# Performance work log

Measured on AMD Instinct MI355X. Metric: run time of the kernel, lower is better.

## Reference

```python
import jax, jax.numpy as jnp
import numpy as np

B, S, D, H = 4, 2048, 512, 8
INNER = D  # assumed AttentionHead.inner_size == size (naive single-head attention)


def setup_inputs() -> dict:
    key = jax.random.key(0)
    ks = jax.random.split(key, 8)
    scale = 0.02
    return {
        "emb_input": jax.random.normal(ks[0], (B, S, D), dtype=jnp.float32),
        "Wq": jax.random.normal(ks[1], (H, D, INNER), dtype=jnp.float32) * scale,
        "bq": jnp.zeros((H, INNER), dtype=jnp.float32),
        "Wk": jax.random.normal(ks[2], (H, D, INNER), dtype=jnp.float32) * scale,
        "bk": jnp.zeros((H, INNER), dtype=jnp.float32),
        "Wv": jax.random.normal(ks[3], (H, D, INNER), dtype=jnp.float32) * scale,
        "bv": jnp.zeros((H, INNER), dtype=jnp.float32),
        "Wp": jax.random.normal(ks[4], (H * INNER, D), dtype=jnp.float32) * scale,
        "bp": jnp.zeros((D,), dtype=jnp.float32),
    }


def reference(emb_input, Wq, bq, Wk, bk, Wv, bv, Wp, bp):
    # All heads batched into one einsum instead of a Python loop over submodules.
    x = emb_input  # [B, S, D]
    q = jnp.einsum("bsd,hde->bhse", x, Wq) + bq[None, :, None, :]  # [B,H,S,E]
    k = jnp.einsum("bsd,hde->bhse", x, Wk) + bk[None, :, None, :]
    v = jnp.einsum("bsd,hde->bhse", x, Wv) + bv[None, :, None, :]
    scores = jnp.einsum("bhse,bhte->bhst", q, k) / jnp.sqrt(
        jnp.asarray(INNER, dtype=x.dtype)
    )  # [B,H,S,S]
    attn = jax.nn.softmax(scores, axis=-1)
    o = jnp.einsum("bhst,bhte->bhse", attn, v)  # [B,H,S,E]
    # concat over heads (dim=2 in torch => feature dim after per-head outputs)
    o = jnp.transpose(o, (0, 2, 1, 3)).reshape(B, S, H * INNER)
    return o @ Wp + bp  # [B, S, D]
```

## Files before the change

kernel.cpp:

```cpp
#include <hip/hip_runtime.h>


typedef short s8v __attribute__((ext_vector_type(8)));
typedef float f4v __attribute__((ext_vector_type(4)));
typedef unsigned short us;
typedef us us4v __attribute__((ext_vector_type(4)));

__device__ inline us f2b(float f) {
  union { float f; unsigned u; } v; v.f = f;
  unsigned r = v.u + 0x7FFFu + ((v.u >> 16) & 1u);
  return (us)(r >> 16);
}

__device__ inline void gld16(const us* g, us* l) {
  __builtin_amdgcn_global_load_lds(
      (const __attribute__((address_space(1))) void*)g,
      (__attribute__((address_space(3))) void*)l, 16, 0, 0);
}

template <int EPI>
__global__ __launch_bounds__(512, 4) void gemm_nt(
    const us* __restrict__ A, int lda, long long sA0, long long sA1,
    const us* __restrict__ Bm, int ldb, long long sB0, long long sB1,
    const float* __restrict__ bias, const float* __restrict__ bias2,
    const float* __restrict__ bias3,
    void* __restrict__ Cv, void* __restrict__ C2, void* __restrict__ C3,
    int ldc, long long sC0, long long sC1,
    int K, float alpha, int L, int sbits) {
  __shared__ us As[2][8192];
  __shared__ us Bs[2][4096];
  const int t = threadIdx.x;
  const int wv = t >> 6, ln = t & 63;
  const int m16 = ln & 15, quad = ln >> 4;

  const int gx = gridDim.x, gxy = gx * gridDim.y;
  const int nblk = gxy * gridDim.z;
  const int flat = blockIdx.x + gx * blockIdx.y + gxy * blockIdx.z;
  int nid = flat;
  if ((nblk & 7) == 0) nid = (flat & 7) * (nblk >> 3) + (flat >> 3);
  const int bz = nid / gxy, rem = nid % gxy;
  const int by = rem / gx, bx = rem % gx;

  const long long row0 = (long long)by * 256;
  const long long col0 = (long long)bx * 128;
  const int zo = bz >> L, zi = bz & ((1 << L) - 1);
  const us* Az = A + zo * sA0 + zi * sA1;
  const us* Bz = Bm + zo * sB0 + zi * sB1;

  int offA[2], offB;
#pragma unroll
  for (int j = 0; j < 2; ++j) {
    const int c = t + 512 * j;
    const int mb = c >> 6, qd = (c >> 4) & 3, mm = c & 15;
    offA[j] = (int)((row0 + mb * 16 + mm) * (long long)lda + qd * 8);
  }
  {
    const int mb = t >> 6, qd = (t >> 4) & 3, mm = t & 15;
    offB = (int)((col0 + mb * 16 + mm) * (long long)ldb + qd * 8);
  }

  f4v acc[4][4];
#pragma unroll
  for (int r = 0; r < 4; ++r)
#pragma unroll
    for (int c = 0; c < 4; ++c) acc[r][c] = (f4v){0.f, 0.f, 0.f, 0.f};

  const int nk = K >> 5;
  const int fo = quad * 16 + m16;
  const int arow = wv & 3, bcol = wv >> 2;

#pragma unroll
  for (int j = 0; j < 2; ++j)
    gld16(Az + offA[j], (us*)As[0] + (512 * j + wv * 64) * 8);
  gld16(Bz + offB, (us*)Bs[0] + (wv * 64) * 8);

  for (int i = 0; i < nk; ++i) {
    __syncthreads();
    const int cur = i & 1;
    if (i + 1 < nk) {
      const int kof = (i + 1) << 5;
#pragma unroll
      for (int j = 0; j < 2; ++j)
        gld16(Az + offA[j] + kof, (us*)As[cur ^ 1] + (512 * j + wv * 64) * 8);
      gld16(Bz + offB + kof, (us*)Bs[cur ^ 1] + (wv * 64) * 8);
    }
    s8v af[4], bf[4];
#pragma unroll
    for (int r = 0; r < 4; ++r)
      af[r] = *(const s8v*)&As[cur][((arow * 4 + r) * 64 + fo) * 8];
#pragma unroll
    for (int c = 0; c < 4; ++c)
      bf[c] = *(const s8v*)&Bs[cur][((bcol * 4 + c) * 64 + fo) * 8];
#pragma unroll
    for (int r = 0; r < 4; ++r)
#pragma unroll
      for (int c = 0; c < 4; ++c)
        acc[r][c] = __builtin_amdgcn_mfma_f32_16x16x32_bf16(af[r], bf[c], acc[r][c], 0, 0, 0);
  }

  if (EPI == 6) {
#pragma unroll
    for (int r = 0; r < 4; ++r)
#pragma unroll
      for (int c = 0; c < 4; ++c)
#pragma unroll
        for (int g = 0; g < 4; ++g)
          acc[r][c][g] = __expf(fmaf(acc[r][c][g], alpha, -4.f));
  }
#pragma unroll
  for (int r = 0; r < 4; ++r) {
    const int inRow = arow * 64 + r * 16 + quad * 4;
    const long long gr0 = row0 + inRow;
#pragma unroll
    for (int c = 0; c < 4; ++c) {
      const long long gc = col0 + bcol * 64 + c * 16 + m16;
      if (EPI == 3) {
        const int which = (int)(gc >> sbits);
        const int gsec = (int)gc & ((1 << sbits) - 1);
        const int hc = gsec >> 9, e = (int)gc & 511;
        const long long slice =
            ((long long)zo * (1 << (sbits - 9)) + hc) * 1048576LL;
        if (which == 0) {
          us* C = (us*)Cv;
          const float bb = bias[gsec];
#pragma unroll
          for (int g = 0; g < 4; ++g)
            C[slice + (gr0 + g) * 512 + e] = f2b(acc[r][c][g] + bb);
        } else if (which == 1) {
          us* C = (us*)C2;
          const float bb = bias2[gsec];
#pragma unroll
          for (int g = 0; g < 4; ++g)
            C[slice + (gr0 + g) * 512 + e] = f2b(acc[r][c][g] + bb);
        } else {
          us* C = (us*)C3;
          const float bb = bias3[gsec];
          us4v pk;
#pragma unroll
          for (int g = 0; g < 4; ++g) pk[g] = f2b(acc[r][c][g] + bb);
          *(us4v*)&C[slice + (long long)e * 2048 + gr0] = pk;
        }
      } else if (EPI == 5) {
        float* C = (float*)Cv + zo * sC0;
        float* p = C + gr0 * ldc + gc;
#pragma unroll
        for (int g = 0; g < 4; ++g)
          atomicAdd(&p[(long long)g * ldc], acc[r][c][g] * alpha);
      } else if (EPI == 6) {
        us* C = (us*)Cv + zo * sC0 + zi * sC1;
#pragma unroll
        for (int g = 0; g < 4; ++g)
          C[(gr0 + g) * (long long)ldc + gc] = f2b(acc[r][c][g]);
      } else {
        us* C = (us*)Cv + zo * sC0 + zi * sC1;
        const float* lrow = (const float*)C2 + (long long)bz * 2048;
#pragma unroll
        for (int g = 0; g < 4; ++g) {
          const float inv = 1.f / lrow[gr0 + g];
          C[(gr0 + g) * (long long)ldc + gc] = f2b(acc[r][c][g] * inv);
        }
      }
    }
    if (EPI == 6) {
      float* lsum = (float*)C2 + (long long)bz * 2048;
#pragma unroll
      for (int g = 0; g < 4; ++g) {
        float s = acc[r][0][g] + acc[r][1][g] + acc[r][2][g] + acc[r][3][g];
        s += __shfl_xor(s, 1, 64);
        s += __shfl_xor(s, 2, 64);
        s += __shfl_xor(s, 4, 64);
        s += __shfl_xor(s, 8, 64);
        if (m16 == 0) atomicAdd(&lsum[gr0 + g], s);
      }
    }
  }
}

__global__ __launch_bounds__(256) void conv_bf16(const float* __restrict__ in,
                                                 us* __restrict__ out, int n4) {
  const int i = blockIdx.x * 256 + threadIdx.x;
  if (i < n4) {
    const float4 f = ((const float4*)in)[i];
    us4v o;
    o[0] = f2b(f.x); o[1] = f2b(f.y); o[2] = f2b(f.z); o[3] = f2b(f.w);
    ((us4v*)out)[i] = o;
  }
}

__global__ __launch_bounds__(256) void conv_transpose(const float* __restrict__ in,
                                                      us* __restrict__ out,
                                                      int R, int C, int Lc,
                                                      int mask, long long sChunk) {
  __shared__ float tile[32][33];
  const int tx = threadIdx.x & 31, ty = threadIdx.x >> 5;
  const int z = blockIdx.z;
  const long long zi = (long long)z * R * C;
  us* dst = out + (long long)(z >> Lc) * sChunk + (long long)(z & mask) * R * C;
  const int r0 = blockIdx.y * 32, c0 = blockIdx.x * 32;
#pragma unroll
  for (int j = 0; j < 4; ++j)
    tile[ty + 8 * j][tx] = in[zi + (long long)(r0 + ty + 8 * j) * C + c0 + tx];
  __syncthreads();
#pragma unroll
  for (int j = 0; j < 4; ++j)
    dst[(long long)(c0 + ty + 8 * j) * R + r0 + tx] = f2b(tile[tx][ty + 8 * j]);
}

__global__ __launch_bounds__(256) void init_out_kernel(float* __restrict__ out,
                                                       const float* __restrict__ bp,
                                                       int total,
                                                       float* __restrict__ lz,
                                                       int lcnt) {
  const int i = blockIdx.x * 256 + threadIdx.x;
  if (i < total) out[i] = bp[i & 511];
  else if (i < total + lcnt) lz[i - total] = 0.f;
}

extern "C" void kernel_launch(void* const* d_in, const int* in_sizes, int n_in,
                              void* d_out, int out_size, void* d_ws, size_t ws_size,
                              hipStream_t stream) {
  constexpr int Bb = 4, S = 2048, D = 512, H = 8, E = 512, HE = 4096;
  const float* x  = (const float*)d_in[0];
  const float* Wq = (const float*)d_in[1];
  const float* bq = (const float*)d_in[2];
  const float* Wk = (const float*)d_in[3];
  const float* bk = (const float*)d_in[4];
  const float* Wv = (const float*)d_in[5];
  const float* bv = (const float*)d_in[6];
  const float* Wp = (const float*)d_in[7];
  const float* bp = (const float*)d_in[8];
  float* out = (float*)d_out;

  const long long SE = (long long)S * E, SS = (long long)S * S;
  const long long SD = (long long)S * D, ED = (long long)E * D;

  us* xh  = (us*)d_ws;
  us* W3  = xh + 4194304;
  us* WpT = W3 + 6291456;
  us* dyn = WpT + 2097152;

  const size_t fixedB = (size_t)(4194304 + 6291456 + 2097152) * 2;
  const size_t lB = (size_t)H * Bb * S * 4;
  int HC = 8;
  while (HC > 1) {
    const size_t need = fixedB + lB +
        (size_t)HC * (3 * (size_t)Bb * SE + (size_t)Bb * SS) * 2;
    if (need <= ws_size) break;
    HC >>= 1;
  }
  const int Lh = (HC == 8) ? 3 : (HC == 4) ? 2 : (HC == 2) ? 1 : 0;
  const int BHC = Bb * HC;
  const int sbits = 9 + Lh;

  us* qh = dyn;
  us* kh = qh + (size_t)BHC * SE;
  us* vT = kh + (size_t)BHC * SE;
  us* sc = vT + (size_t)BHC * SE;
  float* lb = (float*)(sc + (size_t)BHC * SS);
  us* oh = qh;

  const dim3 tb(256), tg(512);
  const int lcnt = H * Bb * S;
  init_out_kernel<<<dim3((Bb * S * D + lcnt + 255) / 256), tb, 0, stream>>>(
      out, bp, Bb * S * D, lb, lcnt);
  conv_bf16<<<dim3(4194304 / 4 / 256), tb, 0, stream>>>(x, xh, 4194304 / 4);
  const long long sChunk = 3LL * HC * ED;
  conv_transpose<<<dim3(16, 16, H), tb, 0, stream>>>(Wq, W3, D, E, Lh, HC - 1, sChunk);
  conv_transpose<<<dim3(16, 16, H), tb, 0, stream>>>(Wk, W3 + HC * ED, D, E, Lh, HC - 1, sChunk);
  conv_transpose<<<dim3(16, 16, H), tb, 0, stream>>>(Wv, W3 + 2 * HC * ED, D, E, Lh, HC - 1, sChunk);
  conv_transpose<<<dim3(16, 128, 1), tb, 0, stream>>>(Wp, WpT, HE, D, 0, 0, 0);

  const float aS = 0.044194173824159216f;
  const dim3 gQKV(3 * HC * E / 128, 8, Bb);
  const dim3 gS(16, 8, BHC);
  const dim3 gPV(4, 8, BHC);
  const dim3 gOP(4, 8, BHC);

  for (int c = 0; c < H / HC; ++c) {
    const int h0 = c * HC;
    float* lc = lb + (long long)c * BHC * S;
    gemm_nt<3><<<gQKV, tg, 0, stream>>>(
        xh, D, SD, 0, W3 + c * sChunk, D, 0, 0,
        bq + h0 * E, bk + h0 * E, bv + h0 * E,
        qh, kh, vT, 512, 0, SE, D, 1.f, 0, sbits);
    gemm_nt<6><<<gS, tg, 0, stream>>>(
        qh, E, (long long)HC * SE, SE, kh, E, (long long)HC * SE, SE,
        nullptr, nullptr, nullptr, sc, lc, nullptr,
        S, (long long)HC * SS, SS, E, aS, Lh, 0);
    gemm_nt<7><<<gPV, tg, 0, stream>>>(
        sc, S, (long long)HC * SS, SS, vT, S, (long long)HC * SE, SE,
        nullptr, nullptr, nullptr, oh, lc, nullptr,
        HC * E, (long long)S * HC * E, E, S, 1.f, Lh, 0);
    gemm_nt<5><<<gOP, tg, 0, stream>>>(
        oh, HC * E, (long long)S * HC * E, 512,
        WpT + (long long)h0 * E, HE, 0, 512,
        nullptr, nullptr, nullptr, out, nullptr, nullptr,
        D, SD, 0, 512, 1.f, Lh, 0);
  }
}
```

Baseline: 951.0 us.

## Use 128x128 four-wave GEMM tiles for attention and fuse prep kernels

Adds a 256-thread GEMM kernel with 128x128 output tiles and moves the score (QK^T with exp) and PV GEMMs onto it, doubling their grid in the row dimension. This gives more blocks and possibly higher occupancy for the attention GEMMs, at the cost of less data reuse per block. It also merges the output/bias init with the x-to-bf16 conversion into one kernel, and the three QKV weight transposes into one launch, to cut launch overhead. The QKV and output-projection GEMMs keep the 512-thread kernel.

```diff
diff --git a/kernel.cpp b/kernel.cpp
--- a/kernel.cpp
+++ b/kernel.cpp
@@ -19,7 +19,127 @@
 }
 
 template <int EPI>
-__global__ __launch_bounds__(512, 4) void gemm_nt(
+__global__ __launch_bounds__(256, 4) void gemm4(
+    const us* __restrict__ A, int lda, long long sA0, long long sA1,
+    const us* __restrict__ Bm, int ldb, long long sB0, long long sB1,
+    void* __restrict__ Cv, float* __restrict__ C2,
+    int ldc, long long sC0, long long sC1,
+    int K, float alpha, int L) {
+  __shared__ us As[2][4096];
+  __shared__ us Bs[2][4096];
+  const int t = threadIdx.x;
+  const int wv = t >> 6, ln = t & 63;
+  const int m16 = ln & 15, quad = ln >> 4;
+
+  const int gx = gridDim.x, gxy = gx * gridDim.y;
+  const int nblk = gxy * gridDim.z;
+  const int flat = blockIdx.x + gx * blockIdx.y + gxy * blockIdx.z;
+  int nid = flat;
+  if ((nblk & 7) == 0) nid = (flat & 7) * (nblk >> 3) + (flat >> 3);
+  const int bz = nid / gxy, rem = nid % gxy;
+  const int by = rem / gx, bx = rem % gx;
+
+  const long long row0 = (long long)by * 128;
+  const long long col0 = (long long)bx * 128;
+  const int zo = bz >> L, zi = bz & ((1 << L) - 1);
+  const us* Az = A + zo * sA0 + zi * sA1;
+  const us* Bz = Bm + zo * sB0 + zi * sB1;
+
+  int offA[2], offB[2];
+#pragma unroll
+  for (int j = 0; j < 2; ++j) {
+    const int c = t + 256 * j;
+    const int mb = c >> 6, qd = (c >> 4) & 3, mm = c & 15;
+    offA[j] = (int)((row0 + mb * 16 + mm) * (long long)lda + qd * 8);
+    offB[j] = (int)((col0 + mb * 16 + mm) * (long long)ldb + qd * 8);
+  }
+
+  f4v acc[4][4];
+#pragma unroll
+  for (int r = 0; r < 4; ++r)
+#pragma unroll
+    for (int c = 0; c < 4; ++c) acc[r][c] = (f4v){0.f, 0.f, 0.f, 0.f};
+
+  const int nk = K >> 5;
+  const int fo = quad * 16 + m16;
+
+#pragma unroll
+  for (int j = 0; j < 2; ++j) {
+    gld16(Az + offA[j], (us*)As[0] + (256 * j + wv * 64) * 8);
+    gld16(Bz + offB[j], (us*)Bs[0] + (256 * j + wv * 64) * 8);
+  }
+
+  for (int i = 0; i < nk; ++i) {
+    __syncthreads();
+    const int cur = i & 1;
+    if (i + 1 < nk) {
+      const int kof = (i + 1) << 5;
+#pragma unroll
+      for (int j = 0; j < 2; ++j) {
+        gld16(Az + offA[j] + kof, (us*)As[cur ^ 1] + (256 * j + wv * 64) * 8);
+        gld16(Bz + offB[j] + kof, (us*)Bs[cur ^ 1] + (256 * j + wv * 64) * 8);
+      }
+    }
+    s8v af[4], bf[4];
+#pragma unroll
+    for (int r = 0; r < 4; ++r)
+      af[r] = *(const s8v*)&As[cur][(((wv & 1) * 4 + r) * 64 + fo) * 8];
+#pragma unroll
+    for (int c = 0; c < 4; ++c)
+      bf[c] = *(const s8v*)&Bs[cur][(((wv >> 1) * 4 + c) * 64 + fo) * 8];
+#pragma unroll
+    for (int r = 0; r < 4; ++r)
+#pragma unroll
+      for (int c = 0; c < 4; ++c)
+        acc[r][c] = __builtin_amdgcn_mfma_f32_16x16x32_bf16(af[r], bf[c], acc[r][c], 0, 0, 0);
+  }
+
+  if (EPI == 6) {
+#pragma unroll
+    for (int r = 0; r < 4; ++r)
+#pragma unroll
+      for (int c = 0; c < 4; ++c)
+#pragma unroll
+        for (int g = 0; g < 4; ++g)
+          acc[r][c][g] = __expf(fmaf(acc[r][c][g], alpha, -4.f));
+  }
+#pragma unroll
+  for (int r = 0; r < 4; ++r) {
+    const long long gr0 = row0 + (wv & 1) * 64 + r * 16 + quad * 4;
+#pragma unroll
+    for (int c = 0; c < 4; ++c) {
+      const long long gc = col0 + (wv >> 1) * 64 + c * 16 + m16;
+      us* C = (us*)Cv + zo * sC0 + zi * sC1;
+      if (EPI == 6) {
+#pragma unroll
+        for (int g = 0; g < 4; ++g)
+          C[(gr0 + g) * (long long)ldc + gc] = f2b(acc[r][c][g]);
+      } else {
+        const float* lrow = C2 + (long long)bz * 2048;
+#pragma unroll
+        for (int g = 0; g < 4; ++g) {
+          const float inv = 1.f / lrow[gr0 + g];
+          C[(gr0 + g) * (long long)ldc + gc] = f2b(acc[r][c][g] * inv);
+        }
+      }
+    }
+    if (EPI == 6) {
+      float* lsum = C2 + (long long)bz * 2048;
+#pragma unroll
+      for (int g = 0; g < 4; ++g) {
+        float s = acc[r][0][g] + acc[r][1][g] + acc[r][2][g] + acc[r][3][g];
+        s += __shfl_xor(s, 1, 64);
+        s += __shfl_xor(s, 2, 64);
+        s += __shfl_xor(s, 4, 64);
+        s += __shfl_xor(s, 8, 64);
+        if (m16 == 0) atomicAdd(&lsum[gr0 + g], s);
+      }
+    }
+  }
+}
+
+template <int EPI>
+__global__ __launch_bounds__(512, 4) void gemm8(
     const us* __restrict__ A, int lda, long long sA0, long long sA1,
     const us* __restrict__ Bm, int ldb, long long sB0, long long sB1,
     const float* __restrict__ bias, const float* __restrict__ bias2,
@@ -98,19 +218,9 @@
         acc[r][c] = __builtin_amdgcn_mfma_f32_16x16x32_bf16(af[r], bf[c], acc[r][c], 0, 0, 0);
   }
 
-  if (EPI == 6) {
-#pragma unroll
-    for (int r = 0; r < 4; ++r)
-#pragma unroll
-      for (int c = 0; c < 4; ++c)
-#pragma unroll
-        for (int g = 0; g < 4; ++g)
-          acc[r][c][g] = __expf(fmaf(acc[r][c][g], alpha, -4.f));
-  }
 #pragma unroll
   for (int r = 0; r < 4; ++r) {
-    const int inRow = arow * 64 + r * 16 + quad * 4;
-    const long long gr0 = row0 + inRow;
+    const long long gr0 = row0 + arow * 64 + r * 16 + quad * 4;
 #pragma unroll
     for (int c = 0; c < 4; ++c) {
       const long long gc = col0 + bcol * 64 + c * 16 + m16;
@@ -140,80 +250,69 @@
           for (int g = 0; g < 4; ++g) pk[g] = f2b(acc[r][c][g] + bb);
           *(us4v*)&C[slice + (long long)e * 2048 + gr0] = pk;
         }
-      } else if (EPI == 5) {
+      } else {
         float* C = (float*)Cv + zo * sC0;
         float* p = C + gr0 * ldc + gc;
 #pragma unroll
         for (int g = 0; g < 4; ++g)
           atomicAdd(&p[(long long)g * ldc], acc[r][c][g] * alpha);
-      } else if (EPI == 6) {
-        us* C = (us*)Cv + zo * sC0 + zi * sC1;
-#pragma unroll
-        for (int g = 0; g < 4; ++g)
-          C[(gr0 + g) * (long long)ldc + gc] = f2b(acc[r][c][g]);
-      } else {
-        us* C = (us*)Cv + zo * sC0 + zi * sC1;
-        const float* lrow = (const float*)C2 + (long long)bz * 2048;
-#pragma unroll
-        for (int g = 0; g < 4; ++g) {
-          const float inv = 1.f / lrow[gr0 + g];
-          C[(gr0 + g) * (long long)ldc + gc] = f2b(acc[r][c][g] * inv);
-        }
       }
     }
-    if (EPI == 6) {
-      float* lsum = (float*)C2 + (long long)bz * 2048;
-#pragma unroll
-      for (int g = 0; g < 4; ++g) {
-        float s = acc[r][0][g] + acc[r][1][g] + acc[r][2][g] + acc[r][3][g];
-        s += __shfl_xor(s, 1, 64);
-        s += __shfl_xor(s, 2, 64);
-        s += __shfl_xor(s, 4, 64);
-        s += __shfl_xor(s, 8, 64);
-        if (m16 == 0) atomicAdd(&lsum[gr0 + g], s);
-      }
-    }
-  }
-}
-
-__global__ __launch_bounds__(256) void conv_bf16(const float* __restrict__ in,
-                                                 us* __restrict__ out, int n4) {
+  }
+}
+
+__global__ __launch_bounds__(256) void prep_kernel(const float* __restrict__ x,
+                                                   us* __restrict__ xh,
+                                                   float* __restrict__ out,
+                                                   const float* __restrict__ bp,
+                                                   float* __restrict__ lz) {
   const int i = blockIdx.x * 256 + threadIdx.x;
-  if (i < n4) {
-    const float4 f = ((const float4*)in)[i];
+  if (i < 4194304) out[i] = bp[i & 511];
+  else if (i < 4194304 + 65536) lz[i - 4194304] = 0.f;
+  if (i < 1048576) {
+    const float4 f = ((const float4*)x)[i];
     us4v o;
     o[0] = f2b(f.x); o[1] = f2b(f.y); o[2] = f2b(f.z); o[3] = f2b(f.w);
-    ((us4v*)out)[i] = o;
-  }
-}
-
-__global__ __launch_bounds__(256) void conv_transpose(const float* __restrict__ in,
-                                                      us* __restrict__ out,
-                                                      int R, int C, int Lc,
-                                                      int mask, long long sChunk) {
+    ((us4v*)xh)[i] = o;
+  }
+}
+
+__global__ __launch_bounds__(256) void convT_qkv(const float* __restrict__ Wq,
+                                                 const float* __restrict__ Wk,
+                                                 const float* __restrict__ Wv,
+                                                 us* __restrict__ W3,
+                                                 int Lh, int mask,
+                                                 long long sChunk) {
   __shared__ float tile[32][33];
   const int tx = threadIdx.x & 31, ty = threadIdx.x >> 5;
   const int z = blockIdx.z;
-  const long long zi = (long long)z * R * C;
-  us* dst = out + (long long)(z >> Lc) * sChunk + (long long)(z & mask) * R * C;
+  const int sec = z >> 3, hd = z & 7;
+  const float* in = (sec == 0 ? Wq : sec == 1 ? Wk : Wv) + (long long)hd * 262144;
+  us* dst = W3 + (long long)(hd >> Lh) * sChunk +
+            (long long)sec * ((long long)(mask + 1) * 262144) +
+            (long long)(hd & mask) * 262144;
   const int r0 = blockIdx.y * 32, c0 = blockIdx.x * 32;
 #pragma unroll
   for (int j = 0; j < 4; ++j)
-    tile[ty + 8 * j][tx] = in[zi + (long long)(r0 + ty + 8 * j) * C + c0 + tx];
+    tile[ty + 8 * j][tx] = in[(long long)(r0 + ty + 8 * j) * 512 + c0 + tx];
   __syncthreads();
 #pragma unroll
   for (int j = 0; j < 4; ++j)
-    dst[(long long)(c0 + ty + 8 * j) * R + r0 + tx] = f2b(tile[tx][ty + 8 * j]);
-}
-
-__global__ __launch_bounds__(256) void init_out_kernel(float* __restrict__ out,
-                                                       const float* __restrict__ bp,
-                                                       int total,
-                                                       float* __restrict__ lz,
-                                                       int lcnt) {
-  const int i = blockIdx.x * 256 + threadIdx.x;
-  if (i < total) out[i] = bp[i & 511];
-  else if (i < total + lcnt) lz[i - total] = 0.f;
+    dst[(long long)(c0 + ty + 8 * j) * 512 + r0 + tx] = f2b(tile[tx][ty + 8 * j]);
+}
+
+__global__ __launch_bounds__(256) void convT_wp(const float* __restrict__ in,
+                                                us* __restrict__ out) {
+  __shared__ float tile[32][33];
+  const int tx = threadIdx.x & 31, ty = threadIdx.x >> 5;
+  const int r0 = blockIdx.y * 32, c0 = blockIdx.x * 32;
+#pragma unroll
+  for (int j = 0; j < 4; ++j)
+    tile[ty + 8 * j][tx] = in[(long long)(r0 + ty + 8 * j) * 512 + c0 + tx];
+  __syncthreads();
+#pragma unroll
+  for (int j = 0; j < 4; ++j)
+    out[(long long)(c0 + ty + 8 * j) * 4096 + r0 + tx] = f2b(tile[tx][ty + 8 * j]);
 }
 
 extern "C" void kernel_launch(void* const* d_in, const int* in_sizes, int n_in,
@@ -260,38 +359,32 @@
   us* oh = qh;
 
   const dim3 tb(256), tg(512);
-  const int lcnt = H * Bb * S;
-  init_out_kernel<<<dim3((Bb * S * D + lcnt + 255) / 256), tb, 0, stream>>>(
-      out, bp, Bb * S * D, lb, lcnt);
-  conv_bf16<<<dim3(4194304 / 4 / 256), tb, 0, stream>>>(x, xh, 4194304 / 4);
+  prep_kernel<<<dim3((4194304 + 65536 + 255) / 256), tb, 0, stream>>>(
+      x, xh, out, bp, lb);
   const long long sChunk = 3LL * HC * ED;
-  conv_transpose<<<dim3(16, 16, H), tb, 0, stream>>>(Wq, W3, D, E, Lh, HC - 1, sChunk);
-  conv_transpose<<<dim3(16, 16, H), tb, 0, stream>>>(Wk, W3 + HC * ED, D, E, Lh, HC - 1, sChunk);
-  conv_transpose<<<dim3(16, 16, H), tb, 0, stream>>>(Wv, W3 + 2 * HC * ED, D, E, Lh, HC - 1, sChunk);
-  conv_transpose<<<dim3(16, 128, 1), tb, 0, stream>>>(Wp, WpT, HE, D, 0, 0, 0);
+  convT_qkv<<<dim3(16, 16, 24), tb, 0, stream>>>(Wq, Wk, Wv, W3, Lh, HC - 1, sChunk);
+  convT_wp<<<dim3(16, 128, 1), tb, 0, stream>>>(Wp, WpT);
 
   const float aS = 0.044194173824159216f;
   const dim3 gQKV(3 * HC * E / 128, 8, Bb);
-  const dim3 gS(16, 8, BHC);
-  const dim3 gPV(4, 8, BHC);
+  const dim3 gS(16, 16, BHC);
+  const dim3 gPV(4, 16, BHC);
   const dim3 gOP(4, 8, BHC);
 
   for (int c = 0; c < H / HC; ++c) {
     const int h0 = c * HC;
     float* lc = lb + (long long)c * BHC * S;
-    gemm_nt<3><<<gQKV, tg, 0, stream>>>(
+    gemm8<3><<<gQKV, tg, 0, stream>>>(
         xh, D, SD, 0, W3 + c * sChunk, D, 0, 0,
         bq + h0 * E, bk + h0 * E, bv + h0 * E,
         qh, kh, vT, 512, 0, SE, D, 1.f, 0, sbits);
-    gemm_nt<6><<<gS, tg, 0, stream>>>(
+    gemm4<6><<<gS, tb, 0, stream>>>(
         qh, E, (long long)HC * SE, SE, kh, E, (long long)HC * SE, SE,
-        nullptr, nullptr, nullptr, sc, lc, nullptr,
-        S, (long long)HC * SS, SS, E, aS, Lh, 0);
-    gemm_nt<7><<<gPV, tg, 0, stream>>>(
+        sc, lc, S, (long long)HC * SS, SS, E, aS, Lh);
+    gemm4<7><<<gPV, tb, 0, stream>>>(
         sc, S, (long long)HC * SS, SS, vT, S, (long long)HC * SE, SE,
-        nullptr, nullptr, nullptr, oh, lc, nullptr,
-        HC * E, (long long)S * HC * E, E, S, 1.f, Lh, 0);
-    gemm_nt<5><<<gOP, tg, 0, stream>>>(
+        oh, lc, HC * E, (long long)S * HC * E, E, S, 1.f, Lh);
+    gemm8<5><<<gOP, tg, 0, stream>>>(
         oh, HC * E, (long long)S * HC * E, 512,
         WpT + (long long)h0 * E, HE, 0, 512,
         nullptr, nullptr, nullptr, out, nullptr, nullptr,
```

Measured after the change: 1.030 ms. 1.08x slower.
